# Kernel optimization log

Hardware: AMD Instinct MI355X
Metric: run time of the kernel (lower is better)

## Reference

```python
import jax, jax.numpy as jnp
import numpy as np

B, T, C = 2, 2048, 2048
N_HEAD, N_GROUPS, HEAD_SIZE = 16, 4, 128
Q_PER_KV = N_HEAD // N_GROUPS  # 4
N_ELEM = HEAD_SIZE  # rotary_percentage = 1.0
HIDDEN = 4 * C
EPS = 1e-5


def layernorm(x, w, b):
    m = jnp.mean(x, axis=-1, keepdims=True)
    v = jnp.mean(jnp.square(x - m), axis=-1, keepdims=True)
    return (x - m) * jax.lax.rsqrt(v + EPS) * w + b


def apply_rope(x, cos, sin):
    # x: [B, H, T, n_elem]; cos/sin: [T, n_elem] (broadcast over B, H)
    d = x.shape[-1]
    x1, x2 = x[..., : d // 2], x[..., d // 2 :]
    rotated = jnp.concatenate((-x2, x1), axis=-1)
    return x * cos + rotated * sin


def setup_inputs() -> dict:
    key = jax.random.key(0)
    ks = jax.random.split(key, 8)
    x = jax.random.normal(ks[0], (B, T, C), dtype=jnp.float32)
    # rope cache (NeoX/LLaMA half-rotation layout), base 10000
    theta = 1.0 / (10000.0 ** (jnp.arange(0, N_ELEM, 2, dtype=jnp.float32) / N_ELEM))
    idx_theta = jnp.outer(jnp.arange(T, dtype=jnp.float32), theta)  # [T, n_elem//2]
    idx_theta = jnp.concatenate((idx_theta, idx_theta), axis=-1)    # [T, n_elem]
    cos, sin = jnp.cos(idx_theta), jnp.sin(idx_theta)
    mask = jnp.tril(jnp.ones((T, T), dtype=bool))[None, None]  # causal [1,1,T,T]
    s = 0.02
    return {
        "x": x,
        "cos": cos,
        "sin": sin,
        "ln1_w": jnp.ones((C,), jnp.float32),
        "ln1_b": jnp.zeros((C,), jnp.float32),
        "ln2_w": jnp.ones((C,), jnp.float32),
        "ln2_b": jnp.zeros((C,), jnp.float32),
        "w_attn": jax.random.normal(ks[1], (C, (N_HEAD + 2 * N_GROUPS) * HEAD_SIZE), jnp.float32) * s,
        "w_proj": jax.random.normal(ks[2], (C, C), jnp.float32) * s,
        "w_fc": jax.random.normal(ks[3], (C, HIDDEN), jnp.float32) * s,
        "w_mlp_proj": jax.random.normal(ks[4], (HIDDEN, C), jnp.float32) * s,
        "mask": mask,
    }


def reference(x, cos, sin, ln1_w, ln1_b, ln2_w, ln2_b, w_attn, w_proj, w_fc, w_mlp_proj, mask):
    n1 = layernorm(x, ln1_w, ln1_b)
    # fused QKV projection
    qkv = n1 @ w_attn  # [B, T, (H + 2G) * hs]
    qkv = qkv.reshape(B, T, N_GROUPS, Q_PER_KV + 2, HEAD_SIZE)
    q = qkv[:, :, :, :Q_PER_KV]      # [B, T, G, qpk, hs]
    k = qkv[:, :, :, Q_PER_KV]       # [B, T, G, hs]
    v = qkv[:, :, :, Q_PER_KV + 1]   # [B, T, G, hs]
    # q -> [B, H, T, hs] (group-major head order)
    q = q.transpose(0, 2, 3, 1, 4).reshape(B, N_HEAD, T, HEAD_SIZE)
    # k, v -> [B, G, T, hs] then repeat_interleave groups to H heads
    k = jnp.repeat(k.transpose(0, 2, 1, 3), Q_PER_KV, axis=1)  # [B, H, T, hs]
    v = jnp.repeat(v.transpose(0, 2, 1, 3), Q_PER_KV, axis=1)
    # RoPE on the first N_ELEM dims (here full head)
    q = jnp.concatenate((apply_rope(q[..., :N_ELEM], cos, sin), q[..., N_ELEM:]), axis=-1)
    k = jnp.concatenate((apply_rope(k[..., :N_ELEM], cos, sin), k[..., N_ELEM:]), axis=-1)
    scale = 1.0 / np.sqrt(HEAD_SIZE).astype(np.float32)
    att = jnp.einsum("bhtd,bhsd->bhts", q, k) * scale
    att = jnp.where(mask, att, jnp.finfo(att.dtype).min)
    att = jax.nn.softmax(att, axis=-1)
    y = jnp.einsum("bhts,bhsd->bhtd", att, v)
    y = y.transpose(0, 2, 1, 3).reshape(B, T, C)
    h = y @ w_proj
    # non-parallel residual (LLaMA-style): x + attn, then x + mlp(norm2(x))
    x = x + h
    n2 = layernorm(x, ln2_w, ln2_b)
    mlp = jax.nn.gelu(n2 @ w_fc, approximate=False) @ w_mlp_proj
    return x + mlp
```

## Files before the change

kernel.cpp:

```cpp
#include <hip/hip_runtime.h>
#include <stdint.h>
#include <math.h>

#define Tn   2048
#define Cn   2048
#define BTn  4096
#define NQKV 3072
#define HID  8192

typedef unsigned short u16;
typedef float f32x4 __attribute__((ext_vector_type(4)));
typedef short s16x8 __attribute__((ext_vector_type(8)));

__device__ __forceinline__ float b2f(u16 u) { return __uint_as_float(((unsigned)u) << 16); }
__device__ __forceinline__ u16 f2b(float f) {
  unsigned i = __float_as_uint(f);
  return (u16)((i + 0x7fffu + ((i >> 16) & 1u)) >> 16);
}

__device__ __forceinline__ void g2l16(const void* g, void* l) {
  __builtin_amdgcn_global_load_lds((const __attribute__((address_space(1))) unsigned int*)g,
                                   (__attribute__((address_space(3))) unsigned int*)l,
                                   16, 0, 0);
}

__global__ __launch_bounds__(256) void transpose_f2b(const float* __restrict__ in,
                                                     u16* __restrict__ out, int R, int C) {
  __shared__ float tile[32][33];
  int bx = blockIdx.x * 32, by = blockIdx.y * 32;
  int tx = threadIdx.x, ty = threadIdx.y;
  #pragma unroll
  for (int j = 0; j < 32; j += 8)
    tile[ty + j][tx] = in[(size_t)(by + ty + j) * C + bx + tx];
  __syncthreads();
  #pragma unroll
  for (int j = 0; j < 32; j += 8)
    out[(size_t)(bx + ty + j) * R + by + tx] = f2b(tile[tx][ty + j]);
}

__global__ __launch_bounds__(256) void transpose_u16(const u16* __restrict__ in,
                                                     u16* __restrict__ out, int R, int C) {
  __shared__ u16 tile[32][33];
  const size_t zb = (size_t)blockIdx.z * R * C;
  int bx = blockIdx.x * 32, by = blockIdx.y * 32;
  int tx = threadIdx.x, ty = threadIdx.y;
  #pragma unroll
  for (int j = 0; j < 32; j += 8)
    tile[ty + j][tx] = in[zb + (size_t)(by + ty + j) * C + bx + tx];
  __syncthreads();
  #pragma unroll
  for (int j = 0; j < 32; j += 8)
    out[zb + (size_t)(bx + ty + j) * R + by + tx] = tile[tx][ty + j];
}

__global__ __launch_bounds__(256)
void copy_f32(const float* __restrict__ in, float* __restrict__ out) {
  const long i = ((long)blockIdx.x * 256 + threadIdx.x) * 4;
  *(f32x4*)(out + i) = *(const f32x4*)(in + i);
}

__global__ __launch_bounds__(256)
void layernorm_k(const float* __restrict__ x, const float* __restrict__ w,
                 const float* __restrict__ bb, u16* __restrict__ out) {
  __shared__ float red[256];
  __shared__ float sm, sv;
  const int tid = threadIdx.x;
  const long row = blockIdx.x;
  const float* xr = x + row * (long)Cn;
  float v[8];
  float s = 0.f;
  #pragma unroll
  for (int i = 0; i < 8; ++i) { v[i] = xr[i * 256 + tid]; s += v[i]; }
  red[tid] = s; __syncthreads();
  for (int st = 128; st > 0; st >>= 1) { if (tid < st) red[tid] += red[tid + st]; __syncthreads(); }
  if (tid == 0) sm = red[0] * (1.f / Cn);
  __syncthreads();
  const float mean = sm;
  float s2 = 0.f;
  #pragma unroll
  for (int i = 0; i < 8; ++i) { float d = v[i] - mean; s2 += d * d; }
  red[tid] = s2; __syncthreads();
  for (int st = 128; st > 0; st >>= 1) { if (tid < st) red[tid] += red[tid + st]; __syncthreads(); }
  if (tid == 0) sv = rsqrtf(red[0] * (1.f / Cn) + 1e-5f);
  __syncthreads();
  const float rstd = sv;
  #pragma unroll
  for (int i = 0; i < 8; ++i) {
    int c = i * 256 + tid;
    out[row * (long)Cn + c] = f2b((v[i] - mean) * rstd * w[c] + bb[c]);
  }
}

__global__ __launch_bounds__(256)
void rope_split(const u16* __restrict__ qkv, const float* __restrict__ cs,
                const float* __restrict__ sn, u16* __restrict__ q,
                u16* __restrict__ k, u16* __restrict__ v) {
  const long idx = (long)blockIdx.x * 256 + threadIdx.x;
  const int row = (int)(idx / NQKV);
  const int col = (int)(idx % NQKV);
  const int b = row >> 11, t = row & 2047;
  const int g = col / 768, rr = col % 768, s = rr >> 7, d = rr & 127;
  const u16 raw = qkv[idx];
  if (s == 5) { v[((long)(b * 4 + g) * Tn + t) * 128 + d] = raw; return; }
  const float xv = b2f(raw);
  const float x2 = b2f(qkv[idx - d + (d ^ 64)]);
  const float c = cs[t * 128 + d];
  const float si = sn[t * 128 + d];
  const float rot = (d < 64) ? -x2 : x2;
  const float o = xv * c + rot * si;
  if (s == 4) k[((long)(b * 4 + g) * Tn + t) * 128 + d] = f2b(o);
  else        q[((long)(b * 16 + g * 4 + s) * Tn + t) * 128 + d] = f2b(o);
}

__global__ __launch_bounds__(256, 2)
void attn_flash(const u16* __restrict__ q, const u16* __restrict__ k,
                const u16* __restrict__ vt, u16* __restrict__ y) {
  __shared__ __align__(16) u16 Ks[4 * 64 * 32];
  __shared__ __align__(16) u16 Vs[2 * 128 * 32];
  __shared__ __align__(16) u16 Ps[4][2 * 16 * 32];
  const int tid = threadIdx.x, wave = tid >> 6, lane = tid & 63;
  const int fr = lane & 15, quad = lane >> 4;
  const int lr4 = lane >> 2, lc8 = (lane & 3) << 3;
  const int bx = blockIdx.x, bh = blockIdx.y;
  const int b = bh >> 4, h = bh & 15, g = h >> 2;
  const int bg = b * 4 + g;
  const u16* kg = k + (size_t)bg * Tn * 128;
  const u16* vg = vt + (size_t)bg * 128 * Tn;
  const int q0 = bx * 64 + wave * 16;

  s16x8 qf[4];
  {
    const u16* qrow = q + ((size_t)bh * Tn + q0 + fr) * 128;
    #pragma unroll
    for (int kc = 0; kc < 4; ++kc)
      qf[kc] = *(const s16x8*)(qrow + kc * 32 + quad * 8);
  }
  f32x4 o_acc[8] = {};
  float m_r[4], l_r[4];
  #pragma unroll
  for (int r = 0; r < 4; ++r) { m_r[r] = -1e30f; l_r[r] = 0.f; }
  const float scale = 0.08838834764831845f;

  for (int step = 0; step <= bx; ++step) {
    const int j0 = step * 64;
    __syncthreads();
    #pragma unroll
    for (int kc = 0; kc < 4; ++kc)
      g2l16(kg + (size_t)(j0 + wave * 16 + lr4) * 128 + kc * 32 + lc8,
            Ks + kc * 2048 + wave * 16 * 32);
    #pragma unroll
    for (int kc = 0; kc < 2; ++kc)
      #pragma unroll
      for (int hh = 0; hh < 2; ++hh)
        g2l16(vg + (size_t)(wave * 32 + hh * 16 + lr4) * Tn + j0 + kc * 32 + lc8,
              Vs + kc * 4096 + (wave * 32 + hh * 16) * 32);
    __syncthreads();

    f32x4 s[4] = {};
    #pragma unroll
    for (int kc = 0; kc < 4; ++kc)
      #pragma unroll
      for (int nt = 0; nt < 4; ++nt) {
        s16x8 bf = *(const s16x8*)(Ks + kc * 2048 + (nt * 16 + fr) * 32 + quad * 8);
        s[nt] = __builtin_amdgcn_mfma_f32_16x16x32_bf16(qf[kc], bf, s[nt], 0, 0, 0);
      }

    const bool diag = (step == bx);
    #pragma unroll
    for (int r = 0; r < 4; ++r) {
      float vmax = -1e30f;
      #pragma unroll
      for (int nt = 0; nt < 4; ++nt) {
        float sv = s[nt][r] * scale;
        if (diag && (j0 + nt * 16 + fr) > (q0 + quad * 4 + r)) sv = -1e30f;
        s[nt][r] = sv;
        vmax = fmaxf(vmax, sv);
      }
      #pragma unroll
      for (int mk = 1; mk < 16; mk <<= 1) vmax = fmaxf(vmax, __shfl_xor(vmax, mk, 64));
      const float mnew = fmaxf(m_r[r], vmax);
      const float alpha = __expf(m_r[r] - mnew);
      float rsum = 0.f;
      #pragma unroll
      for (int nt = 0; nt < 4; ++nt) {
        float pv = __expf(s[nt][r] - mnew);
        s[nt][r] = pv; rsum += pv;
      }
      #pragma unroll
      for (int mk = 1; mk < 16; mk <<= 1) rsum += __shfl_xor(rsum, mk, 64);
      l_r[r] = l_r[r] * alpha + rsum;
      m_r[r] = mnew;
      #pragma unroll
      for (int nt = 0; nt < 8; ++nt) o_acc[nt][r] *= alpha;
    }

    u16* pw = Ps[wave];
    #pragma unroll
    for (int nt = 0; nt < 4; ++nt) {
      const int col = nt * 16 + fr, pan = col >> 5, cc = col & 31;
      #pragma unroll
      for (int r = 0; r < 4; ++r)
        pw[pan * 512 + (quad * 4 + r) * 32 + cc] = f2b(s[nt][r]);
    }
    #pragma unroll
    for (int kc = 0; kc < 2; ++kc) {
      s16x8 af = *(const s16x8*)(pw + kc * 512 + fr * 32 + quad * 8);
      #pragma unroll
      for (int nt = 0; nt < 8; ++nt) {
        s16x8 bf = *(const s16x8*)(Vs + kc * 4096 + (nt * 16 + fr) * 32 + quad * 8);
        o_acc[nt] = __builtin_amdgcn_mfma_f32_16x16x32_bf16(af, bf, o_acc[nt], 0, 0, 0);
      }
    }
  }

  #pragma unroll
  for (int r = 0; r < 4; ++r) {
    const float inv = 1.f / l_r[r];
    const size_t row = (size_t)(b * Tn + q0 + quad * 4 + r) * Cn + h * 128;
    #pragma unroll
    for (int nt = 0; nt < 8; ++nt)
      y[row + nt * 16 + fr] = f2b(o_acc[nt][r] * inv);
  }
}

#define BAR  __builtin_amdgcn_s_barrier()
#define LG0  asm volatile("s_waitcnt lgkmcnt(0)" ::: "memory")
#define RD_A(BUF, MI4)                                                                  \
  { _Pragma("unroll") for (int m_ = 0; m_ < 4; ++m_) {                                  \
      _Pragma("unroll") for (int k_ = 0; k_ < 2; ++k_)                                  \
        ar[m_][k_] = *(const s16x8*)(Sb + (BUF) * 32768 + aBase +                       \
                                     (((MI4) + m_) << 11) + (k_ << 10) + fragoff); } }
#define RD_B(BUF, NI2, DST)                                                             \
  { _Pragma("unroll") for (int n_ = 0; n_ < 2; ++n_) {                                  \
      _Pragma("unroll") for (int k_ = 0; k_ < 2; ++k_)                                  \
        DST[n_][k_] = *(const s16x8*)(Sb + (BUF) * 32768 + bBase +                      \
                                      (((NI2) + n_) << 11) + (k_ << 10) + fragoff); } }
#define MM(MB, NB, BR)                                                                  \
  { __builtin_amdgcn_s_setprio(1);                                                     \
    _Pragma("unroll") for (int m_ = 0; m_ < 4; ++m_) {                                  \
      _Pragma("unroll") for (int n_ = 0; n_ < 2; ++n_) {                                \
        _Pragma("unroll") for (int k_ = 0; k_ < 2; ++k_)                                \
          acc[(MB) + m_][(NB) + n_] = __builtin_amdgcn_mfma_f32_16x16x32_bf16(          \
              ar[m_][k_], BR[n_][k_], acc[(MB) + m_][(NB) + n_], 0, 0, 0); } }          \
    __builtin_amdgcn_s_setprio(0); }

template <int EPI>
__global__ __launch_bounds__(512, 2)
void gemm256(const u16* __restrict__ A, const u16* __restrict__ Bt,
             const float* __restrict__ res, u16* __restrict__ ob,
             float* __restrict__ of, int N, int Kl, int ld, int num_n) {
  __shared__ __align__(16) u16 S[65536];
  char* Sb = (char*)S;

  const long koff = (long)blockIdx.y * Kl;
  A += koff; Bt += koff;

  const int pid = blockIdx.x;
  const int xcd = pid & 7, idx = pid >> 3;
  const int jj = idx & 3;
  const int gp = (idx >> 2) * 8 + xcd;
  const int npc = num_n >> 1;
  const int pr = gp / npc, pc = gp - pr * npc;
  const long m0 = (long)(pr * 2 + (jj >> 1)) * 256;
  const long n0 = (long)(pc * 2 + (jj & 1)) * 256;

  const int tid = (int)threadIdx.x;
  const int wave = tid >> 6, lane = tid & 63;
  const int wr = wave >> 2, wc = wave & 3;
  const int fr = lane & 15, quad = lane >> 4;
  const int fragoff = (fr * 64 + quad * 16) ^ (((fr >> 3) & 1) << 5);
  const int aBase = wr * 16384;
  const int bBase = 65536 + (wc >> 1) * 16384 + ((wc & 1) << 13);

  int srow[2], skcb[2];
  #pragma unroll
  for (int rr = 0; rr < 2; ++rr) {
    const int d = rr * 8192 + wave * 1024 + lane * 16;
    const int l = d ^ (((d >> 9) & 1) << 5);
    srow[rr] = ((l >> 11) << 4) | ((l >> 6) & 15);
    skcb[rr] = (((l >> 10) & 1) << 6) | (l & 63);
  }
  auto stage = [&](const u16* __restrict__ src, long grow0, int kt, int regionByte) {
    #pragma unroll
    for (int rr = 0; rr < 2; ++rr)
      g2l16((const char*)src + (grow0 + srow[rr]) * (long)ld * 2 + (long)kt * 128 + skcb[rr],
            Sb + regionByte + rr * 8192 + wave * 1024);
  };

  const int nk = Kl >> 6;
  const int nk2 = nk >> 1;

  stage(A,  m0,       0, 0);
  stage(A,  m0 + 128, 0, 16384);
  stage(Bt, n0,       0, 65536);
  stage(Bt, n0 + 128, 0, 81920);
  stage(Bt, n0,       1, 98304);
  stage(Bt, n0 + 128, 1, 114688);
  asm volatile("s_waitcnt vmcnt(4)" ::: "memory");
  BAR;

  s16x8 ar[4][2], br0[2][2], br1[2][2];
  f32x4 acc[8][4] = {};

  for (int i = 0; i < nk2; ++i) {
    const int t1 = 2 * i + 1, s0 = 2 * i + 2, s1 = 2 * i + 3;
    const bool v0 = (s0 < nk), v1 = (s1 < nk);
    RD_A(0, 0); RD_B(0, 0, br0);
    stage(A, m0, t1, 32768);
    LG0; MM(0, 0, br0); BAR;
    RD_B(0, 2, br1);
    stage(A, m0 + 128, t1, 49152);
    LG0; MM(0, 2, br1); BAR;
    RD_A(0, 4);
    if (v0) stage(Bt, n0, s0, 65536);
    LG0; MM(4, 2, br1); BAR;
    if (v0) stage(Bt, n0 + 128, s0, 81920);
    MM(4, 0, br0);
    if (v0) { asm volatile("s_waitcnt vmcnt(4)" ::: "memory"); }
    else    { asm volatile("s_waitcnt vmcnt(0)" ::: "memory"); }
    BAR;
    RD_A(1, 0); RD_B(1, 0, br0);
    if (v0) stage(A, m0, s0, 0);
    LG0; MM(0, 0, br0); BAR;
    RD_B(1, 2, br1);
    if (v0) stage(A, m0 + 128, s0, 16384);
    LG0; MM(0, 2, br1); BAR;
    RD_A(1, 4);
    if (v1) stage(Bt, n0, s1, 98304);
    LG0; MM(4, 2, br1); BAR;
    if (v1) stage(Bt, n0 + 128, s1, 114688);
    MM(4, 0, br0);
    asm volatile("s_waitcnt vmcnt(4)" ::: "memory");
    BAR;
  }

  #pragma unroll
  for (int mi = 0; mi < 8; ++mi)
    #pragma unroll
    for (int ni = 0; ni < 4; ++ni)
      #pragma unroll
      for (int r = 0; r < 4; ++r) {
        const long row = m0 + wr * 128 + mi * 16 + quad * 4 + r;
        const long col = n0 + wc * 64 + ni * 16 + fr;
        const long idx2 = row * N + col;
        const float vv = acc[mi][ni][r];
        if (EPI == 0) ob[idx2] = f2b(vv);
        else if (EPI == 1) of[idx2] = vv + res[idx2];
        else if (EPI == 2) ob[idx2] = f2b(0.5f * vv * (1.0f + erff(vv * 0.70710678118654752f)));
        else atomicAdd(&of[idx2], vv);
      }
}

extern "C" void kernel_launch(void* const* d_in, const int* in_sizes, int n_in,
                              void* d_out, int out_size, void* d_ws, size_t ws_size,
                              hipStream_t stream) {
  (void)in_sizes; (void)n_in; (void)out_size; (void)ws_size;
  const float* x      = (const float*)d_in[0];
  const float* cosb   = (const float*)d_in[1];
  const float* sinb   = (const float*)d_in[2];
  const float* ln1w   = (const float*)d_in[3];
  const float* ln1b   = (const float*)d_in[4];
  const float* ln2w   = (const float*)d_in[5];
  const float* ln2b   = (const float*)d_in[6];
  const float* w_attn = (const float*)d_in[7];
  const float* w_proj = (const float*)d_in[8];
  const float* w_fc   = (const float*)d_in[9];
  const float* w_mp   = (const float*)d_in[10];
  float* out = (float*)d_out;

  char* p = (char*)d_ws;
  auto alloc = [&](size_t bytes) { char* r = p; p += (bytes + 255) & ~(size_t)255; return (void*)r; };
  u16*  wT_attn = (u16*)alloc((size_t)NQKV * Cn * 2);
  u16*  wT_proj = (u16*)alloc((size_t)Cn * Cn * 2);
  u16*  wT_fc   = (u16*)alloc((size_t)HID * Cn * 2);
  u16*  wT_mp   = (u16*)alloc((size_t)Cn * HID * 2);
  u16*  n12     = (u16*)alloc((size_t)BTn * Cn * 2);
  u16*  qkv     = (u16*)alloc((size_t)BTn * NQKV * 2);
  u16*  qb      = (u16*)alloc((size_t)2 * 16 * Tn * 128 * 2);
  u16*  kb      = (u16*)alloc((size_t)2 * 4 * Tn * 128 * 2);
  u16*  vb      = (u16*)alloc((size_t)2 * 4 * Tn * 128 * 2);
  float* x1     = (float*)alloc((size_t)BTn * Cn * 4);
  u16*  hbuf    = (u16*)alloc((size_t)BTn * HID * 2);
  u16*  vt      = n12;

  dim3 tb(32, 8);
  transpose_f2b<<<dim3(NQKV / 32, Cn / 32), tb, 0, stream>>>(w_attn, wT_attn, Cn, NQKV);
  transpose_f2b<<<dim3(Cn / 32, Cn / 32), tb, 0, stream>>>(w_proj, wT_proj, Cn, Cn);
  transpose_f2b<<<dim3(HID / 32, Cn / 32), tb, 0, stream>>>(w_fc, wT_fc, Cn, HID);
  transpose_f2b<<<dim3(Cn / 32, HID / 32), tb, 0, stream>>>(w_mp, wT_mp, HID, Cn);

  layernorm_k<<<BTn, 256, 0, stream>>>(x, ln1w, ln1b, n12);
  gemm256<0><<<(BTn / 256) * (NQKV / 256), 512, 0, stream>>>(n12, wT_attn, nullptr, qkv, nullptr, NQKV, Cn, Cn, NQKV / 256);
  rope_split<<<(int)(((long)BTn * NQKV) / 256), 256, 0, stream>>>(qkv, cosb, sinb, qb, kb, vb);
  transpose_u16<<<dim3(128 / 32, Tn / 32, 8), tb, 0, stream>>>(vb, vt, Tn, 128);
  attn_flash<<<dim3(Tn / 64, 32), 256, 0, stream>>>(qb, kb, vt, qkv );
  copy_f32<<<(int)(((long)BTn * Cn) / 1024), 256, 0, stream>>>(x, x1);
  gemm256<3><<<dim3((BTn / 256) * (Cn / 256), 2), 512, 0, stream>>>(qkv, wT_proj, nullptr, nullptr, x1, Cn, Cn / 2, Cn, Cn / 256);
  layernorm_k<<<BTn, 256, 0, stream>>>(x1, ln2w, ln2b, n12);
  gemm256<2><<<(BTn / 256) * (HID / 256), 512, 0, stream>>>(n12, wT_fc, nullptr, hbuf, nullptr, HID, Cn, Cn, HID / 256);
  copy_f32<<<(int)(((long)BTn * Cn) / 1024), 256, 0, stream>>>(x1, out);
  gemm256<3><<<dim3((BTn / 256) * (Cn / 256), 2), 512, 0, stream>>>(hbuf, wT_mp, nullptr, nullptr, out, Cn, HID / 2, HID, Cn / 256);
}
```

Before: 883.4 us.

## Double-buffer K/V tiles in flash attention with swizzled LDS layout

The attention kernel now prefetches the next K/V tile into a second LDS buffer while computing on the current one, replacing the two per-step __syncthreads with a single wait plus barrier at the end of each step. It also XOR-swizzles the LDS column slot for K, V and P reads and writes to reduce bank conflicts, and raises wave priority around the MFMA loops. This doubles K/V shared memory per block, which may reduce occupancy, and the swizzle must stay consistent between the staging writes and the fragment reads.

```diff
diff --git a/kernel.cpp b/kernel.cpp
--- a/kernel.cpp
+++ b/kernel.cpp
@@ -115,12 +115,16 @@
 __global__ __launch_bounds__(256, 2)
 void attn_flash(const u16* __restrict__ q, const u16* __restrict__ k,
                 const u16* __restrict__ vt, u16* __restrict__ y) {
-  __shared__ __align__(16) u16 Ks[4 * 64 * 32];
-  __shared__ __align__(16) u16 Vs[2 * 128 * 32];
+  __shared__ __align__(16) u16 Ks[2 * 8192];
+  __shared__ __align__(16) u16 Vs[2 * 8192];
   __shared__ __align__(16) u16 Ps[4][2 * 16 * 32];
   const int tid = threadIdx.x, wave = tid >> 6, lane = tid & 63;
   const int fr = lane & 15, quad = lane >> 4;
-  const int lr4 = lane >> 2, lc8 = (lane & 3) << 3;
+  const int lr4 = lane >> 2;
+  const int su  = ((lr4 >> 3) & 1) << 1;
+  const int lcs = (((lane & 3) ^ su) << 3);
+  const int ksw = ((fr >> 3) & 1) << 1;
+  const int rslot = (quad ^ ksw) << 3;
   const int bx = blockIdx.x, bh = blockIdx.y;
   const int b = bh >> 4, h = bh & 15, g = h >> 2;
   const int bg = b * 4 + g;
@@ -141,29 +145,42 @@
   for (int r = 0; r < 4; ++r) { m_r[r] = -1e30f; l_r[r] = 0.f; }
   const float scale = 0.08838834764831845f;
 
+  auto stage_kv = [&](int j0, int bufsel) {
+    u16* kd = Ks + bufsel * 8192;
+    u16* vd = Vs + bufsel * 8192;
+    #pragma unroll
+    for (int kc = 0; kc < 4; ++kc)
+      g2l16(kg + (size_t)(j0 + wave * 16 + lr4) * 128 + kc * 32 + lcs,
+            kd + kc * 2048 + wave * 512);
+    #pragma unroll
+    for (int kc = 0; kc < 2; ++kc)
+      #pragma unroll
+      for (int hh = 0; hh < 2; ++hh)
+        g2l16(vg + (size_t)(wave * 32 + hh * 16 + lr4) * Tn + j0 + kc * 32 + lcs,
+              vd + kc * 4096 + (wave * 32 + hh * 16) * 32);
+  };
+
+  stage_kv(0, 0);
+  asm volatile("s_waitcnt vmcnt(0)" ::: "memory");
+  __builtin_amdgcn_s_barrier();
+
+  int cur = 0;
   for (int step = 0; step <= bx; ++step) {
     const int j0 = step * 64;
-    __syncthreads();
+    if (step < bx) stage_kv(j0 + 64, cur ^ 1);
+    const u16* kcur = Ks + cur * 8192;
+    const u16* vcur = Vs + cur * 8192;
+
+    f32x4 s[4] = {};
+    __builtin_amdgcn_s_setprio(1);
     #pragma unroll
     for (int kc = 0; kc < 4; ++kc)
-      g2l16(kg + (size_t)(j0 + wave * 16 + lr4) * 128 + kc * 32 + lc8,
-            Ks + kc * 2048 + wave * 16 * 32);
-    #pragma unroll
-    for (int kc = 0; kc < 2; ++kc)
-      #pragma unroll
-      for (int hh = 0; hh < 2; ++hh)
-        g2l16(vg + (size_t)(wave * 32 + hh * 16 + lr4) * Tn + j0 + kc * 32 + lc8,
-              Vs + kc * 4096 + (wave * 32 + hh * 16) * 32);
-    __syncthreads();
-
-    f32x4 s[4] = {};
-    #pragma unroll
-    for (int kc = 0; kc < 4; ++kc)
       #pragma unroll
       for (int nt = 0; nt < 4; ++nt) {
-        s16x8 bf = *(const s16x8*)(Ks + kc * 2048 + (nt * 16 + fr) * 32 + quad * 8);
+        s16x8 bf = *(const s16x8*)(kcur + kc * 2048 + (nt * 16 + fr) * 32 + rslot);
         s[nt] = __builtin_amdgcn_mfma_f32_16x16x32_bf16(qf[kc], bf, s[nt], 0, 0, 0);
       }
+    __builtin_amdgcn_s_setprio(0);
 
     const bool diag = (step == bx);
     #pragma unroll
@@ -199,18 +216,26 @@
     for (int nt = 0; nt < 4; ++nt) {
       const int col = nt * 16 + fr, pan = col >> 5, cc = col & 31;
       #pragma unroll
-      for (int r = 0; r < 4; ++r)
-        pw[pan * 512 + (quad * 4 + r) * 32 + cc] = f2b(s[nt][r]);
+      for (int r = 0; r < 4; ++r) {
+        const int prow = quad * 4 + r;
+        pw[pan * 512 + prow * 32 + (cc ^ (((prow >> 3) & 1) << 4))] = f2b(s[nt][r]);
+      }
     }
     #pragma unroll
     for (int kc = 0; kc < 2; ++kc) {
-      s16x8 af = *(const s16x8*)(pw + kc * 512 + fr * 32 + quad * 8);
+      s16x8 af = *(const s16x8*)(pw + kc * 512 + fr * 32 + rslot);
+      __builtin_amdgcn_s_setprio(1);
       #pragma unroll
       for (int nt = 0; nt < 8; ++nt) {
-        s16x8 bf = *(const s16x8*)(Vs + kc * 4096 + (nt * 16 + fr) * 32 + quad * 8);
+        s16x8 bf = *(const s16x8*)(vcur + kc * 4096 + (nt * 16 + fr) * 32 + rslot);
         o_acc[nt] = __builtin_amdgcn_mfma_f32_16x16x32_bf16(af, bf, o_acc[nt], 0, 0, 0);
       }
+      __builtin_amdgcn_s_setprio(0);
     }
+
+    asm volatile("s_waitcnt vmcnt(0) lgkmcnt(0)" ::: "memory");
+    __builtin_amdgcn_s_barrier();
+    cur ^= 1;
   }
 
   #pragma unroll
```

New measurement: 890.2 us. About the same (+0.8%).
